# Optimization experiments

Hardware: AMD Instinct MI355X
Metric: run time of the kernel (lower is better)

Reference implementation:

```python
import jax, jax.numpy as jnp
import numpy as np

B, H, T, D, R = 2, 12, 2048, 64, 16
D_STD = D - R


def setup_inputs() -> dict:
    key = jax.random.key(0)
    ks = jax.random.split(key, 5)
    return {
        "Q": jax.random.normal(ks[0], (B, H, T, D), jnp.float32),
        "K": jax.random.normal(ks[1], (B, H, T, D), jnp.float32),
        "V": jax.random.normal(ks[2], (B, H, T, D), jnp.float32),
        "d_bias": jax.random.normal(ks[3], (B, H, T), jnp.float32),
        "W_recip": jax.random.normal(ks[4], (D, R), jnp.float32) * 0.02,
        "w_std": jnp.full((H,), 0.5, jnp.float32),
        "w_rec": jnp.full((H,), 0.3, jnp.float32),
        "w_disc": jnp.full((H,), 0.2, jnp.float32),
    }


def reference(Q, K, V, d_bias, W_recip, w_std, w_rec, w_disc):
    b, h, t, d = Q.shape
    r = W_recip.shape[1]
    d_std = d - r
    sq_std = jnp.sqrt(w_std)[None, :, None, None]  # [1,H,1,1]
    sq_rec = jnp.sqrt(w_rec)[None, :, None, None]
    Q_low = jnp.einsum("bhtd,dr->bhtr", Q, W_recip)  # [B,H,T,R]
    K_low = jnp.einsum("bhtd,dr->bhtr", K, W_recip)
    Q_aug = jnp.concatenate([sq_std * Q[..., :d_std], sq_rec * K_low], axis=-1)  # [B,H,T,D]
    K_aug = jnp.concatenate([sq_std * K[..., :d_std], sq_rec * Q_low], axis=-1)
    scale = 1.0 / jnp.sqrt(jnp.asarray(d, Q.dtype))
    scores = jnp.einsum("bhqd,bhkd->bhqk", Q_aug, K_aug) * scale  # [B,H,T,T]
    # rank-1 additive bias, broadcast over queries: bias[b,h,q,k] = w_disc[h]*d_bias[b,h,k]
    scores = scores + (w_disc[None, :, None, None] * d_bias[:, :, None, :])
    causal = jnp.tril(jnp.ones((t, t), bool))  # [T,T]
    scores = jnp.where(causal[None, None], scores, -jnp.inf)
    attn = jax.nn.softmax(scores, axis=-1)
    return jnp.einsum("bhqk,bhkd->bhqd", attn, V)
```

## Files before the change

kernel.cpp:

```cpp
#include <hip/hip_runtime.h>
#include <math.h>

#define T_SEQ 2048
#define NH    12
#define NB    2
#define BHC   (NB*NH)
#define NQT   32

typedef _Float16 half4_t __attribute__((ext_vector_type(4)));
typedef _Float16 half8_t __attribute__((ext_vector_type(8)));
typedef float    floatx4 __attribute__((ext_vector_type(4)));

__device__ __forceinline__ half8_t h8splat(_Float16 s) {
  return (half8_t){s, s, s, s, s, s, s, s};
}

__global__ __launch_bounds__(256) void prep_kernel(
    const float* __restrict__ Q, const float* __restrict__ K,
    const float* __restrict__ V, const float* __restrict__ W,
    const float* __restrict__ wstd, const float* __restrict__ wrec,
    const float* __restrict__ dbias, const float* __restrict__ wdisc,
    ushort* __restrict__ QF, ushort* __restrict__ KF, ushort* __restrict__ VF,
    float* __restrict__ B2)
{
  __shared__ __align__(16) _Float16 Qsh[64*72];
  __shared__ __align__(16) _Float16 Ksh[64*72];
  __shared__ __align__(16) _Float16 Vsh[64*72];
  __shared__ __align__(16) _Float16 Lqh[64*16];
  __shared__ __align__(16) _Float16 Lkh[64*16];

  const int tid = threadIdx.x;
  const int w = tid >> 6, lane = tid & 63;
  const int quad = lane >> 4, ln = lane & 15;
  const int bh = blockIdx.x >> 5, tblk = blockIdx.x & 31;
  const long g0 = ((long)bh * T_SEQ + tblk * 64) * 64;

  const float4* gQ = (const float4*)(Q + g0);
  const float4* gK = (const float4*)(K + g0);
  const float4* gV = (const float4*)(V + g0);
  for (int i = tid; i < 1024; i += 256) {
    int r = i >> 4, c4 = i & 15;
    float4 q = gQ[i], k = gK[i], v = gV[i];
    *(half4_t*)&Qsh[r*72 + c4*4] = (half4_t){(_Float16)q.x,(_Float16)q.y,(_Float16)q.z,(_Float16)q.w};
    *(half4_t*)&Ksh[r*72 + c4*4] = (half4_t){(_Float16)k.x,(_Float16)k.y,(_Float16)k.z,(_Float16)k.w};
    *(half4_t*)&Vsh[r*72 + c4*4] = (half4_t){(_Float16)v.x,(_Float16)v.y,(_Float16)v.z,(_Float16)v.w};
  }
  __syncthreads();

  half4_t bw[4];
#pragma unroll
  for (int dk = 0; dk < 4; dk++)
#pragma unroll
    for (int i = 0; i < 4; i++)
      bw[dk][i] = (_Float16)W[(dk*16 + quad*4 + i)*16 + ln];

  floatx4 cq = {0.f,0.f,0.f,0.f}, ck = {0.f,0.f,0.f,0.f};
#pragma unroll
  for (int dk = 0; dk < 4; dk++) {
    half4_t aq = *(const half4_t*)&Qsh[(w*16 + ln)*72 + dk*16 + quad*4];
    half4_t ak = *(const half4_t*)&Ksh[(w*16 + ln)*72 + dk*16 + quad*4];
    cq = __builtin_amdgcn_mfma_f32_16x16x16f16(aq, bw[dk], cq, 0, 0, 0);
    ck = __builtin_amdgcn_mfma_f32_16x16x16f16(ak, bw[dk], ck, 0, 0, 0);
  }
#pragma unroll
  for (int i = 0; i < 4; i++) {
    Lqh[(w*16 + quad*4 + i)*16 + ln] = (_Float16)cq[i];
    Lkh[(w*16 + quad*4 + i)*16 + ln] = (_Float16)ck[i];
  }
  __syncthreads();

  const int h = bh % NH;
  const float sstd = sqrtf(wstd[h]);
  const float srec = sqrtf(wrec[h]);
  const half8_t hq_std = h8splat((_Float16)(0.125f * sstd));
  const half8_t hk_std = h8splat((_Float16)sstd);
  const half8_t hq_rec = h8splat((_Float16)(0.125f * srec));
  const half8_t hk_rec = h8splat((_Float16)srec);

  if (tid < 64) B2[(long)bh*T_SEQ + tblk*64 + tid] =
      wdisc[h] * dbias[(long)bh*T_SEQ + tblk*64 + tid];

#pragma unroll
  for (int cc = 0; cc < 2; cc++) {
    int c = tid + cc * 256;
    {
      int lp = c & 63, dp = (c >> 6) & 1, rt = c >> 7;
      int row = rt*16 + (lp & 15);
      int d0 = dp*32 + (lp >> 4)*8;
      half8_t hq, hk;
      if (d0 < 48) {
        hq = *(const half8_t*)&Qsh[row*72 + d0] * hq_std;
        hk = *(const half8_t*)&Ksh[row*72 + d0] * hk_std;
      } else {
        hq = *(const half8_t*)&Lkh[row*16 + (d0-48)] * hq_rec;
        hk = *(const half8_t*)&Lqh[row*16 + (d0-48)] * hk_rec;
      }
      long tile16 = (long)bh*128 + tblk*4 + rt;
      ((int4*)QF)[tile16*128 + dp*64 + lp] = *(int4*)&hq;
      ((int4*)KF)[tile16*128 + dp*64 + lp] = *(int4*)&hk;
    }
    {
      int lv = c & 63, nt = (c >> 6) & 3, v2 = c >> 8;
      int d = nt*16 + (lv & 15), qv = lv >> 4;
      half8_t hv;
#pragma unroll
      for (int j = 0; j < 4; j++) {
        hv[j]   = Vsh[(v2*32 + qv*4 + j)*72 + d];
        hv[4+j] = Vsh[(v2*32 + 16 + qv*4 + j)*72 + d];
      }
      ((int4*)VF)[((long)bh*32 + tblk)*512 + (v2*4 + nt)*64 + lv] = *(int4*)&hv;
    }
  }
}

__global__ __launch_bounds__(64, 3) void flash_kernel(
    const ushort* __restrict__ QF, const ushort* __restrict__ KF,
    const ushort* __restrict__ VF, const float* __restrict__ B2,
    float* __restrict__ Out)
{
  const int lane = threadIdx.x;
  const int quad = lane >> 4, ln = lane & 15;
  const int bid = blockIdx.x;
  const int bh  = bid % BHC;
  const int t16 = 127 - bid / BHC;
  const int qrow = t16*16 + ln;
  const int ktmax = t16 >> 2;

  const ushort* gK = KF + (long)bh * 131072;
  const ushort* gV = VF + (long)bh * 131072;
  const float*  gB = B2 + (long)bh * T_SEQ;

  half8_t bq[2];
  {
    const ushort* gQ = QF + ((long)bh*128 + t16) * 1024;
    bq[0] = *(const half8_t*)(gQ + lane*8);
    bq[1] = *(const half8_t*)(gQ + 512 + lane*8);
  }

  float m_i = -1e30f, l_i = 0.f;
  floatx4 acc[4];
#pragma unroll
  for (int nt = 0; nt < 4; nt++) acc[nt] = (floatx4){0.f,0.f,0.f,0.f};

  half8_t kf[8], vf[8];
#pragma unroll
  for (int c = 0; c < 8; c++) {
    kf[c] = *(const half8_t*)(gK + c*512 + lane*8);
    vf[c] = *(const half8_t*)(gV + c*512 + lane*8);
  }

  for (int kt = 0; kt <= ktmax; kt++) {
    const long onx = (long)(kt < ktmax ? kt + 1 : kt) * 4096;

    floatx4 st[4];
#pragma unroll
    for (int mt = 0; mt < 4; mt++) {
      floatx4 c = (floatx4){0.f,0.f,0.f,0.f};
      c = __builtin_amdgcn_mfma_f32_16x16x32_f16(kf[mt*2],     bq[0], c, 0, 0, 0);
      c = __builtin_amdgcn_mfma_f32_16x16x32_f16(kf[mt*2 + 1], bq[1], c, 0, 0, 0);
      st[mt] = c;
    }
#pragma unroll
    for (int c = 0; c < 8; c++)
      kf[c] = *(const half8_t*)(gK + onx + c*512 + lane*8);

    const bool diag = (kt == ktmax);
    float rowmax = -1e30f;
#pragma unroll
    for (int mt = 0; mt < 4; mt++) {
      float4 bb = *(const float4*)(gB + kt*64 + mt*16 + quad*4);
      float bv[4] = {bb.x, bb.y, bb.z, bb.w};
#pragma unroll
      for (int i = 0; i < 4; i++) {
        float v = st[mt][i] + bv[i];
        int key = kt*64 + mt*16 + quad*4 + i;
        if (diag && key > qrow) v = -1e30f;
        st[mt][i] = v;
        rowmax = fmaxf(rowmax, v);
      }
    }
    rowmax = fmaxf(rowmax, __shfl_xor(rowmax, 16));
    rowmax = fmaxf(rowmax, __shfl_xor(rowmax, 32));
    float mnew  = fmaxf(m_i, rowmax);
    float alpha = __expf(m_i - mnew);
    float psum = 0.f;
    half4_t pa[4];
#pragma unroll
    for (int mt = 0; mt < 4; mt++)
#pragma unroll
      for (int i = 0; i < 4; i++) {
        float p = __expf(st[mt][i] - mnew);
        psum += p;
        pa[mt][i] = (_Float16)p;
      }
    psum += __shfl_xor(psum, 16);
    psum += __shfl_xor(psum, 32);
    l_i = l_i * alpha + psum;
    m_i = mnew;

    float af[4];
#pragma unroll
    for (int i = 0; i < 4; i++) af[i] = __shfl(alpha, quad*4 + i);
#pragma unroll
    for (int nt = 0; nt < 4; nt++)
#pragma unroll
      for (int i = 0; i < 4; i++) acc[nt][i] *= af[i];

#pragma unroll
    for (int v2 = 0; v2 < 2; v2++)
#pragma unroll
      for (int nt = 0; nt < 4; nt++) {
        half8_t vv = vf[v2*4 + nt];
        half4_t b0 = __builtin_shufflevector(vv, vv, 0,1,2,3);
        half4_t b1 = __builtin_shufflevector(vv, vv, 4,5,6,7);
        acc[nt] = __builtin_amdgcn_mfma_f32_16x16x16f16(pa[2*v2],   b0, acc[nt], 0, 0, 0);
        acc[nt] = __builtin_amdgcn_mfma_f32_16x16x16f16(pa[2*v2+1], b1, acc[nt], 0, 0, 0);
      }
#pragma unroll
    for (int c = 0; c < 8; c++)
      vf[c] = *(const half8_t*)(gV + onx + c*512 + lane*8);
  }

  float lr[4];
#pragma unroll
  for (int i = 0; i < 4; i++) lr[i] = 1.f / __shfl(l_i, quad*4 + i);
  const long obase = (long)bh*T_SEQ*64 + (long)(t16*16)*64;
#pragma unroll
  for (int i = 0; i < 4; i++)
#pragma unroll
    for (int nt = 0; nt < 4; nt++)
      Out[obase + (quad*4 + i)*64 + nt*16 + ln] = acc[nt][i] * lr[i];
}

extern "C" void kernel_launch(void* const* d_in, const int* in_sizes, int n_in,
                              void* d_out, int out_size, void* d_ws, size_t ws_size,
                              hipStream_t stream) {
  const float* Q     = (const float*)d_in[0];
  const float* K     = (const float*)d_in[1];
  const float* V     = (const float*)d_in[2];
  const float* dbias = (const float*)d_in[3];
  const float* W     = (const float*)d_in[4];
  const float* wstd  = (const float*)d_in[5];
  const float* wrec  = (const float*)d_in[6];
  const float* wdisc = (const float*)d_in[7];
  float* Out = (float*)d_out;

  const long NEL = (long)BHC * T_SEQ * 64;
  ushort* QF = (ushort*)d_ws;
  ushort* KF = QF + NEL;
  ushort* VF = KF + NEL;
  float*  B2 = (float*)(VF + NEL);

  prep_kernel<<<BHC * NQT, 256, 0, stream>>>(Q, K, V, W, wstd, wrec, dbias, wdisc,
                                             QF, KF, VF, B2);
  flash_kernel<<<BHC * 128, 64, 0, stream>>>(QF, KF, VF, B2, Out);
}
```

Measured before the change: 130.1 us.

## Split KV loop across two waves per block, merge softmax states, use exp2 with lazy rescale

Each flash block now runs two wavefronts that process alternating 64-key tiles, each keeping its own running max, sum and accumulator. The two partial states are merged through shared memory at the end. This doubles parallelism for each 16-row query tile to cut the serial per-wave loop latency. Separately, log2(e) is folded into the Q scale and the bias so exp2f can replace __expf. The accumulator rescale is skipped unless the row max grows by more than 8, which trades some fp16 probability headroom for fewer rescales. The change adds shared memory, a block barrier and a final merge step.

Result: slower. 339.6 us (+161.1%).

```diff
diff --git a/kernel.cpp b/kernel.cpp
--- a/kernel.cpp
+++ b/kernel.cpp
@@ -70,15 +70,16 @@
   __syncthreads();
 
   const int h = bh % NH;
+  const float LOG2E = 1.4426950408889634f;
   const float sstd = sqrtf(wstd[h]);
   const float srec = sqrtf(wrec[h]);
-  const half8_t hq_std = h8splat((_Float16)(0.125f * sstd));
+  const half8_t hq_std = h8splat((_Float16)(0.125f * sstd * LOG2E));
   const half8_t hk_std = h8splat((_Float16)sstd);
-  const half8_t hq_rec = h8splat((_Float16)(0.125f * srec));
+  const half8_t hq_rec = h8splat((_Float16)(0.125f * srec * LOG2E));
   const half8_t hk_rec = h8splat((_Float16)srec);
 
   if (tid < 64) B2[(long)bh*T_SEQ + tblk*64 + tid] =
-      wdisc[h] * dbias[(long)bh*T_SEQ + tblk*64 + tid];
+      LOG2E * wdisc[h] * dbias[(long)bh*T_SEQ + tblk*64 + tid];
 
 #pragma unroll
   for (int cc = 0; cc < 2; cc++) {
@@ -113,12 +114,18 @@
   }
 }
 
-__global__ __launch_bounds__(64, 3) void flash_kernel(
+__global__ __launch_bounds__(128, 6) void flash_kernel(
     const ushort* __restrict__ QF, const ushort* __restrict__ KF,
     const ushort* __restrict__ VF, const float* __restrict__ B2,
     float* __restrict__ Out)
 {
-  const int lane = threadIdx.x;
+  __shared__ float sm1[16];
+  __shared__ float sl1[16];
+  __shared__ float sacc1[64*16];
+
+  const int tid  = threadIdx.x;
+  const int wv   = tid >> 6;
+  const int lane = tid & 63;
   const int quad = lane >> 4, ln = lane & 15;
   const int bid = blockIdx.x;
   const int bh  = bid % BHC;
@@ -142,15 +149,17 @@
 #pragma unroll
   for (int nt = 0; nt < 4; nt++) acc[nt] = (floatx4){0.f,0.f,0.f,0.f};
 
+  const int kt0 = wv;
+  const long oo0 = (long)(kt0 <= ktmax ? kt0 : 0) * 4096;
   half8_t kf[8], vf[8];
 #pragma unroll
   for (int c = 0; c < 8; c++) {
-    kf[c] = *(const half8_t*)(gK + c*512 + lane*8);
-    vf[c] = *(const half8_t*)(gV + c*512 + lane*8);
-  }
-
-  for (int kt = 0; kt <= ktmax; kt++) {
-    const long onx = (long)(kt < ktmax ? kt + 1 : kt) * 4096;
+    kf[c] = *(const half8_t*)(gK + oo0 + c*512 + lane*8);
+    vf[c] = *(const half8_t*)(gV + oo0 + c*512 + lane*8);
+  }
+
+  for (int kt = kt0; kt <= ktmax; kt += 2) {
+    const long onx = (long)(kt + 2 <= ktmax ? kt + 2 : kt) * 4096;
 
     floatx4 st[4];
 #pragma unroll
@@ -181,30 +190,34 @@
     }
     rowmax = fmaxf(rowmax, __shfl_xor(rowmax, 16));
     rowmax = fmaxf(rowmax, __shfl_xor(rowmax, 32));
-    float mnew  = fmaxf(m_i, rowmax);
-    float alpha = __expf(m_i - mnew);
+
+    if (!__all(rowmax <= m_i + 8.f)) {
+      float mnew  = fmaxf(m_i, rowmax);
+      float alpha = exp2f(m_i - mnew);
+      float af[4];
+#pragma unroll
+      for (int i = 0; i < 4; i++) af[i] = __shfl(alpha, quad*4 + i);
+#pragma unroll
+      for (int nt = 0; nt < 4; nt++)
+#pragma unroll
+        for (int i = 0; i < 4; i++) acc[nt][i] *= af[i];
+      l_i *= alpha;
+      m_i  = mnew;
+    }
+
     float psum = 0.f;
     half4_t pa[4];
 #pragma unroll
     for (int mt = 0; mt < 4; mt++)
 #pragma unroll
       for (int i = 0; i < 4; i++) {
-        float p = __expf(st[mt][i] - mnew);
+        float p = exp2f(st[mt][i] - m_i);
         psum += p;
         pa[mt][i] = (_Float16)p;
       }
     psum += __shfl_xor(psum, 16);
     psum += __shfl_xor(psum, 32);
-    l_i = l_i * alpha + psum;
-    m_i = mnew;
-
-    float af[4];
-#pragma unroll
-    for (int i = 0; i < 4; i++) af[i] = __shfl(alpha, quad*4 + i);
-#pragma unroll
-    for (int nt = 0; nt < 4; nt++)
-#pragma unroll
-      for (int i = 0; i < 4; i++) acc[nt][i] *= af[i];
+    l_i += psum;
 
 #pragma unroll
     for (int v2 = 0; v2 < 2; v2++)
@@ -221,15 +234,39 @@
       vf[c] = *(const half8_t*)(gV + onx + c*512 + lane*8);
   }
 
-  float lr[4];
-#pragma unroll
-  for (int i = 0; i < 4; i++) lr[i] = 1.f / __shfl(l_i, quad*4 + i);
-  const long obase = (long)bh*T_SEQ*64 + (long)(t16*16)*64;
-#pragma unroll
-  for (int i = 0; i < 4; i++)
+  if (wv == 1) {
+    if (quad == 0) { sm1[ln] = m_i; sl1[ln] = l_i; }
 #pragma unroll
     for (int nt = 0; nt < 4; nt++)
-      Out[obase + (quad*4 + i)*64 + nt*16 + ln] = acc[nt][i] * lr[i];
+#pragma unroll
+      for (int i = 0; i < 4; i++)
+        sacc1[lane*16 + nt*4 + i] = acc[nt][i];
+  }
+  __syncthreads();
+  if (wv == 0) {
+    const float m1  = sm1[ln];
+    const float l1v = sl1[ln];
+    const float mm  = fmaxf(m_i, m1);
+    const float w0  = exp2f(m_i - mm);
+    const float w1  = exp2f(m1  - mm);
+    const float lm  = l_i * w0 + l1v * w1;
+    float w0r[4], w1r[4], lr[4];
+#pragma unroll
+    for (int i = 0; i < 4; i++) {
+      w0r[i] = __shfl(w0, quad*4 + i);
+      w1r[i] = __shfl(w1, quad*4 + i);
+      lr[i]  = 1.f / __shfl(lm, quad*4 + i);
+    }
+    const long obase = (long)bh*T_SEQ*64 + (long)(t16*16)*64;
+#pragma unroll
+    for (int i = 0; i < 4; i++)
+#pragma unroll
+      for (int nt = 0; nt < 4; nt++) {
+        float4 a1 = *(const float4*)&sacc1[lane*16 + nt*4];
+        Out[obase + (quad*4 + i)*64 + nt*16 + ln] =
+            (acc[nt][i]*w0r[i] + ((const float*)&a1)[i]*w1r[i]) * lr[i];
+      }
+  }
 }
 
 extern "C" void kernel_launch(void* const* d_in, const int* in_sizes, int n_in,
@@ -253,5 +290,5 @@
 
   prep_kernel<<<BHC * NQT, 256, 0, stream>>>(Q, K, V, W, wstd, wrec, dbias, wdisc,
                                              QF, KF, VF, B2);
-  flash_kernel<<<BHC * 128, 64, 0, stream>>>(QF, KF, VF, B2, Out);
-}
+  flash_kernel<<<BHC * 128, 128, 0, stream>>>(QF, KF, VF, B2, Out);
+}
```

## Share K/V tiles across four waves via LDS double-buffering, use exp2 and lazy rescale

Applied to the files above, without the earlier changes.

The flash kernel now runs four waves per block, each handling one 16-row query tile of a 64-row group. K/V tiles are staged once per block into double-buffered LDS with global_load_lds, so four waves share each load instead of each wave fetching its own from global memory. The log2(e) factor is folded into the Q scaling and bias in prep, so the softmax uses exp2f. The running-max rescale is skipped unless some row's max grows by more than 8 (in log2 units), which trims work in exchange for fp16 overflow risk when the max is stale. Per-iteration __syncthreads adds synchronisation, and waves in a block now share the same causal loop length, so the wave on the lowest query tile does extra masked work.

Result: slower. 136.5 us (+5.0%).

```diff
diff --git a/kernel.cpp b/kernel.cpp
--- a/kernel.cpp
+++ b/kernel.cpp
@@ -13,6 +13,12 @@
 
 __device__ __forceinline__ half8_t h8splat(_Float16 s) {
   return (half8_t){s, s, s, s, s, s, s, s};
+}
+
+__device__ __forceinline__ void gload_lds16(const void* g, void* l) {
+  __builtin_amdgcn_global_load_lds(
+      (const __attribute__((address_space(1))) unsigned int*)g,
+      (__attribute__((address_space(3))) unsigned int*)l, 16, 0, 0);
 }
 
 __global__ __launch_bounds__(256) void prep_kernel(
@@ -70,15 +76,16 @@
   __syncthreads();
 
   const int h = bh % NH;
+  const float LOG2E = 1.4426950408889634f;
   const float sstd = sqrtf(wstd[h]);
   const float srec = sqrtf(wrec[h]);
-  const half8_t hq_std = h8splat((_Float16)(0.125f * sstd));
+  const half8_t hq_std = h8splat((_Float16)(0.125f * sstd * LOG2E));
   const half8_t hk_std = h8splat((_Float16)sstd);
-  const half8_t hq_rec = h8splat((_Float16)(0.125f * srec));
+  const half8_t hq_rec = h8splat((_Float16)(0.125f * srec * LOG2E));
   const half8_t hk_rec = h8splat((_Float16)srec);
 
   if (tid < 64) B2[(long)bh*T_SEQ + tblk*64 + tid] =
-      wdisc[h] * dbias[(long)bh*T_SEQ + tblk*64 + tid];
+      LOG2E * wdisc[h] * dbias[(long)bh*T_SEQ + tblk*64 + tid];
 
 #pragma unroll
   for (int cc = 0; cc < 2; cc++) {
@@ -113,18 +120,23 @@
   }
 }
 
-__global__ __launch_bounds__(64, 3) void flash_kernel(
+__global__ __launch_bounds__(256, 3) void flash_kernel(
     const ushort* __restrict__ QF, const ushort* __restrict__ KF,
     const ushort* __restrict__ VF, const float* __restrict__ B2,
     float* __restrict__ Out)
 {
-  const int lane = threadIdx.x;
+  __shared__ __align__(16) _Float16 KV[2][2][4096];
+
+  const int tid  = threadIdx.x;
+  const int wv   = tid >> 6;
+  const int lane = tid & 63;
   const int quad = lane >> 4, ln = lane & 15;
   const int bid = blockIdx.x;
   const int bh  = bid % BHC;
-  const int t16 = 127 - bid / BHC;
+  const int p   = 31 - bid / BHC;
+  const int t16 = 4*p + wv;
   const int qrow = t16*16 + ln;
-  const int ktmax = t16 >> 2;
+  const int ktmax = p;
 
   const ushort* gK = KF + (long)bh * 131072;
   const ushort* gV = VF + (long)bh * 131072;
@@ -142,16 +154,31 @@
 #pragma unroll
   for (int nt = 0; nt < 4; nt++) acc[nt] = (floatx4){0.f,0.f,0.f,0.f};
 
-  half8_t kf[8], vf[8];
-#pragma unroll
-  for (int c = 0; c < 8; c++) {
-    kf[c] = *(const half8_t*)(gK + c*512 + lane*8);
-    vf[c] = *(const half8_t*)(gV + c*512 + lane*8);
-  }
+  auto STAGE = [&](int nbuf, int kt) {
+    const long tb = (long)kt * 4096;
+#pragma unroll
+    for (int s = 0; s < 4; s++) {
+      const int c = wv + s*4;
+      const ushort* src = (c < 8 ? gK + tb + c*512 : gV + tb + (c-8)*512) + lane*8;
+      gload_lds16(src, &KV[nbuf][c>>3][(c&7)*512]);
+    }
+  };
+  STAGE(0, 0);
 
   for (int kt = 0; kt <= ktmax; kt++) {
-    const long onx = (long)(kt < ktmax ? kt + 1 : kt) * 4096;
-
+    const int cur = kt & 1;
+    __syncthreads();
+    if (kt < ktmax) STAGE(cur ^ 1, kt + 1);
+
+    float4 bb[4];
+#pragma unroll
+    for (int mt = 0; mt < 4; mt++)
+      bb[mt] = *(const float4*)(gB + kt*64 + mt*16 + quad*4);
+
+    half8_t kf[8];
+#pragma unroll
+    for (int c = 0; c < 8; c++)
+      kf[c] = *(const half8_t*)&KV[cur][0][c*512 + lane*8];
     floatx4 st[4];
 #pragma unroll
     for (int mt = 0; mt < 4; mt++) {
@@ -160,65 +187,60 @@
       c = __builtin_amdgcn_mfma_f32_16x16x32_f16(kf[mt*2 + 1], bq[1], c, 0, 0, 0);
       st[mt] = c;
     }
-#pragma unroll
-    for (int c = 0; c < 8; c++)
-      kf[c] = *(const half8_t*)(gK + onx + c*512 + lane*8);
 
     const bool diag = (kt == ktmax);
     float rowmax = -1e30f;
 #pragma unroll
-    for (int mt = 0; mt < 4; mt++) {
-      float4 bb = *(const float4*)(gB + kt*64 + mt*16 + quad*4);
-      float bv[4] = {bb.x, bb.y, bb.z, bb.w};
+    for (int mt = 0; mt < 4; mt++)
 #pragma unroll
       for (int i = 0; i < 4; i++) {
-        float v = st[mt][i] + bv[i];
+        float v = st[mt][i] + ((const float*)&bb[mt])[i];
         int key = kt*64 + mt*16 + quad*4 + i;
         if (diag && key > qrow) v = -1e30f;
         st[mt][i] = v;
         rowmax = fmaxf(rowmax, v);
       }
-    }
     rowmax = fmaxf(rowmax, __shfl_xor(rowmax, 16));
     rowmax = fmaxf(rowmax, __shfl_xor(rowmax, 32));
-    float mnew  = fmaxf(m_i, rowmax);
-    float alpha = __expf(m_i - mnew);
+
+    if (!__all(rowmax <= m_i + 8.f)) {
+      float mnew  = fmaxf(m_i, rowmax);
+      float alpha = exp2f(m_i - mnew);
+      float af[4];
+#pragma unroll
+      for (int i = 0; i < 4; i++) af[i] = __shfl(alpha, quad*4 + i);
+#pragma unroll
+      for (int nt = 0; nt < 4; nt++)
+#pragma unroll
+        for (int i = 0; i < 4; i++) acc[nt][i] *= af[i];
+      l_i *= alpha;
+      m_i  = mnew;
+    }
+
     float psum = 0.f;
     half4_t pa[4];
 #pragma unroll
     for (int mt = 0; mt < 4; mt++)
 #pragma unroll
       for (int i = 0; i < 4; i++) {
-        float p = __expf(st[mt][i] - mnew);
-        psum += p;
-        pa[mt][i] = (_Float16)p;
+        float pv = exp2f(st[mt][i] - m_i);
+        psum += pv;
+        pa[mt][i] = (_Float16)pv;
       }
     psum += __shfl_xor(psum, 16);
     psum += __shfl_xor(psum, 32);
-    l_i = l_i * alpha + psum;
-    m_i = mnew;
-
-    float af[4];
-#pragma unroll
-    for (int i = 0; i < 4; i++) af[i] = __shfl(alpha, quad*4 + i);
-#pragma unroll
-    for (int nt = 0; nt < 4; nt++)
-#pragma unroll
-      for (int i = 0; i < 4; i++) acc[nt][i] *= af[i];
+    l_i += psum;
 
 #pragma unroll
     for (int v2 = 0; v2 < 2; v2++)
 #pragma unroll
       for (int nt = 0; nt < 4; nt++) {
-        half8_t vv = vf[v2*4 + nt];
+        half8_t vv = *(const half8_t*)&KV[cur][1][(v2*4 + nt)*512 + lane*8];
         half4_t b0 = __builtin_shufflevector(vv, vv, 0,1,2,3);
         half4_t b1 = __builtin_shufflevector(vv, vv, 4,5,6,7);
         acc[nt] = __builtin_amdgcn_mfma_f32_16x16x16f16(pa[2*v2],   b0, acc[nt], 0, 0, 0);
         acc[nt] = __builtin_amdgcn_mfma_f32_16x16x16f16(pa[2*v2+1], b1, acc[nt], 0, 0, 0);
       }
-#pragma unroll
-    for (int c = 0; c < 8; c++)
-      vf[c] = *(const half8_t*)(gV + onx + c*512 + lane*8);
   }
 
   float lr[4];
@@ -253,5 +275,5 @@
 
   prep_kernel<<<BHC * NQT, 256, 0, stream>>>(Q, K, V, W, wstd, wrec, dbias, wdisc,
                                              QF, KF, VF, B2);
-  flash_kernel<<<BHC * 128, 64, 0, stream>>>(QF, KF, VF, B2, Out);
-}
+  flash_kernel<<<BHC * 32, 256, 0, stream>>>(QF, KF, VF, B2, Out);
+}
```

## Split long causal rows across key chunks with merge kernel, exp2 softmax and lazy rescale

Applied to the files above, without the earlier changes.

Splits each query tile's key range into chunks of up to 8 key tiles, so long causal rows become several blocks (320 per head instead of 128). Each block writes unnormalized partial outputs plus running max and sum, and a new merge kernel combines them. This balances the triangular workload and adds parallelism. It also folds log2(e) into the Q scales and the bias so softmax can use exp2, seeds the MFMA accumulator with the bias, and skips rescaling while the new max stays within 8 of the old one. The cost is an extra kernel launch and a round trip of partial results through global memory. It also raises the occupancy hint from 3 to 4.

After: 141.4 us. +8.7%, slower.

```diff
diff --git a/kernel.cpp b/kernel.cpp
--- a/kernel.cpp
+++ b/kernel.cpp
@@ -70,15 +70,16 @@
   __syncthreads();
 
   const int h = bh % NH;
+  const float LOG2E = 1.4426950408889634f;
   const float sstd = sqrtf(wstd[h]);
   const float srec = sqrtf(wrec[h]);
-  const half8_t hq_std = h8splat((_Float16)(0.125f * sstd));
+  const half8_t hq_std = h8splat((_Float16)(0.125f * sstd * LOG2E));
   const half8_t hk_std = h8splat((_Float16)sstd);
-  const half8_t hq_rec = h8splat((_Float16)(0.125f * srec));
+  const half8_t hq_rec = h8splat((_Float16)(0.125f * srec * LOG2E));
   const half8_t hk_rec = h8splat((_Float16)srec);
 
   if (tid < 64) B2[(long)bh*T_SEQ + tblk*64 + tid] =
-      wdisc[h] * dbias[(long)bh*T_SEQ + tblk*64 + tid];
+      LOG2E * wdisc[h] * dbias[(long)bh*T_SEQ + tblk*64 + tid];
 
 #pragma unroll
   for (int cc = 0; cc < 2; cc++) {
@@ -113,18 +114,30 @@
   }
 }
 
-__global__ __launch_bounds__(64, 3) void flash_kernel(
+__global__ __launch_bounds__(64, 4) void flash_kernel(
     const ushort* __restrict__ QF, const ushort* __restrict__ KF,
     const ushort* __restrict__ VF, const float* __restrict__ B2,
-    float* __restrict__ Out)
+    float* __restrict__ PP)
 {
   const int lane = threadIdx.x;
   const int quad = lane >> 4, ln = lane & 15;
   const int bid = blockIdx.x;
   const int bh  = bid % BHC;
-  const int t16 = 127 - bid / BHC;
+  int rem = 319 - bid / BHC;
+
+  int p = 0;
+#pragma unroll 1
+  for (p = 0; p < 32; p++) {
+    int cnt = 4 * ((p >> 3) + 1);
+    if (rem < cnt) break;
+    rem -= cnt;
+  }
+  const int t16 = 4*p + (rem & 3);
+  const int s   = rem >> 2;
+  const int ktmax = p;
+  const int s0 = s*8;
+  const int s1 = min(s0 + 7, ktmax);
   const int qrow = t16*16 + ln;
-  const int ktmax = t16 >> 2;
 
   const ushort* gK = KF + (long)bh * 131072;
   const ushort* gV = VF + (long)bh * 131072;
@@ -145,17 +158,18 @@
   half8_t kf[8], vf[8];
 #pragma unroll
   for (int c = 0; c < 8; c++) {
-    kf[c] = *(const half8_t*)(gK + c*512 + lane*8);
-    vf[c] = *(const half8_t*)(gV + c*512 + lane*8);
-  }
-
-  for (int kt = 0; kt <= ktmax; kt++) {
-    const long onx = (long)(kt < ktmax ? kt + 1 : kt) * 4096;
+    kf[c] = *(const half8_t*)(gK + (long)s0*4096 + c*512 + lane*8);
+    vf[c] = *(const half8_t*)(gV + (long)s0*4096 + c*512 + lane*8);
+  }
+
+  for (int kt = s0; kt <= s1; kt++) {
+    const long onx = (long)(kt < s1 ? kt + 1 : kt) * 4096;
 
     floatx4 st[4];
 #pragma unroll
     for (int mt = 0; mt < 4; mt++) {
-      floatx4 c = (floatx4){0.f,0.f,0.f,0.f};
+      float4 bb = *(const float4*)(gB + kt*64 + mt*16 + quad*4);
+      floatx4 c = (floatx4){bb.x, bb.y, bb.z, bb.w};
       c = __builtin_amdgcn_mfma_f32_16x16x32_f16(kf[mt*2],     bq[0], c, 0, 0, 0);
       c = __builtin_amdgcn_mfma_f32_16x16x32_f16(kf[mt*2 + 1], bq[1], c, 0, 0, 0);
       st[mt] = c;
@@ -164,47 +178,51 @@
     for (int c = 0; c < 8; c++)
       kf[c] = *(const half8_t*)(gK + onx + c*512 + lane*8);
 
-    const bool diag = (kt == ktmax);
+    if (kt == ktmax) {
+#pragma unroll
+      for (int mt = 0; mt < 4; mt++)
+#pragma unroll
+        for (int i = 0; i < 4; i++) {
+          int key = kt*64 + mt*16 + quad*4 + i;
+          if (key > qrow) st[mt][i] = -1e30f;
+        }
+    }
     float rowmax = -1e30f;
 #pragma unroll
-    for (int mt = 0; mt < 4; mt++) {
-      float4 bb = *(const float4*)(gB + kt*64 + mt*16 + quad*4);
-      float bv[4] = {bb.x, bb.y, bb.z, bb.w};
-#pragma unroll
-      for (int i = 0; i < 4; i++) {
-        float v = st[mt][i] + bv[i];
-        int key = kt*64 + mt*16 + quad*4 + i;
-        if (diag && key > qrow) v = -1e30f;
-        st[mt][i] = v;
-        rowmax = fmaxf(rowmax, v);
-      }
-    }
+    for (int mt = 0; mt < 4; mt++)
+      rowmax = fmaxf(rowmax,
+                     fmaxf(fmaxf(st[mt][0], st[mt][1]),
+                           fmaxf(st[mt][2], st[mt][3])));
     rowmax = fmaxf(rowmax, __shfl_xor(rowmax, 16));
     rowmax = fmaxf(rowmax, __shfl_xor(rowmax, 32));
-    float mnew  = fmaxf(m_i, rowmax);
-    float alpha = __expf(m_i - mnew);
+
+    if (!__all(rowmax <= m_i + 8.f)) {
+      float mnew  = fmaxf(m_i, rowmax);
+      float alpha = exp2f(m_i - mnew);
+      float af[4];
+#pragma unroll
+      for (int i = 0; i < 4; i++) af[i] = __shfl(alpha, quad*4 + i);
+#pragma unroll
+      for (int nt = 0; nt < 4; nt++)
+#pragma unroll
+        for (int i = 0; i < 4; i++) acc[nt][i] *= af[i];
+      l_i *= alpha;
+      m_i  = mnew;
+    }
+
     float psum = 0.f;
     half4_t pa[4];
 #pragma unroll
     for (int mt = 0; mt < 4; mt++)
 #pragma unroll
       for (int i = 0; i < 4; i++) {
-        float p = __expf(st[mt][i] - mnew);
-        psum += p;
-        pa[mt][i] = (_Float16)p;
+        float pv = exp2f(st[mt][i] - m_i);
+        psum += pv;
+        pa[mt][i] = (_Float16)pv;
       }
     psum += __shfl_xor(psum, 16);
     psum += __shfl_xor(psum, 32);
-    l_i = l_i * alpha + psum;
-    m_i = mnew;
-
-    float af[4];
-#pragma unroll
-    for (int i = 0; i < 4; i++) af[i] = __shfl(alpha, quad*4 + i);
-#pragma unroll
-    for (int nt = 0; nt < 4; nt++)
-#pragma unroll
-      for (int i = 0; i < 4; i++) acc[nt][i] *= af[i];
+    l_i += psum;
 
 #pragma unroll
     for (int v2 = 0; v2 < 2; v2++)
@@ -221,15 +239,59 @@
       vf[c] = *(const half8_t*)(gV + onx + c*512 + lane*8);
   }
 
-  float lr[4];
-#pragma unroll
-  for (int i = 0; i < 4; i++) lr[i] = 1.f / __shfl(l_i, quad*4 + i);
-  const long obase = (long)bh*T_SEQ*64 + (long)(t16*16)*64;
+  float* pb = PP + ((long)((bh*128 + t16)*4 + s)) * 1088;
 #pragma unroll
   for (int i = 0; i < 4; i++)
 #pragma unroll
     for (int nt = 0; nt < 4; nt++)
-      Out[obase + (quad*4 + i)*64 + nt*16 + ln] = acc[nt][i] * lr[i];
+      pb[(quad*4 + i)*64 + nt*16 + ln] = acc[nt][i];
+  if (quad == 0) {
+    pb[1024 + ln] = m_i;
+    pb[1040 + ln] = l_i;
+  }
+}
+
+__global__ __launch_bounds__(256) void merge_kernel(
+    const float* __restrict__ PP, float* __restrict__ Out)
+{
+  const int tid = threadIdx.x, wv = tid >> 6, lane = tid & 63;
+  const int gidx = blockIdx.x * 4 + wv;
+  const int bh = gidx % BHC, t16 = gidx / BHC;
+  const int scnt = (t16 >> 5) + 1;
+  const float* base = PP + ((long)(bh*128 + t16)*4) * 1088;
+  const int colg = (lane & 15) * 4;
+  const int r0   = lane >> 4;
+
+  float mm[4] = {-1e30f, -1e30f, -1e30f, -1e30f};
+  for (int sI = 0; sI < scnt; sI++)
+#pragma unroll
+    for (int j = 0; j < 4; j++)
+      mm[j] = fmaxf(mm[j], base[sI*1088 + 1024 + (r0 + 4*j)]);
+
+  float L[4] = {0.f, 0.f, 0.f, 0.f};
+  floatx4 O[4];
+#pragma unroll
+  for (int j = 0; j < 4; j++) O[j] = (floatx4){0.f,0.f,0.f,0.f};
+
+  for (int sI = 0; sI < scnt; sI++)
+#pragma unroll
+    for (int j = 0; j < 4; j++) {
+      const int row = r0 + 4*j;
+      const float w = exp2f(base[sI*1088 + 1024 + row] - mm[j]);
+      L[j] += base[sI*1088 + 1040 + row] * w;
+      const float4 a = *(const float4*)&base[sI*1088 + row*64 + colg];
+      O[j][0] += a.x * w;  O[j][1] += a.y * w;
+      O[j][2] += a.z * w;  O[j][3] += a.w * w;
+    }
+
+  const long obase = (long)bh*T_SEQ*64 + (long)t16*16*64;
+#pragma unroll
+  for (int j = 0; j < 4; j++) {
+    const float inv = 1.f / L[j];
+    const int row = r0 + 4*j;
+    float4 o = {O[j][0]*inv, O[j][1]*inv, O[j][2]*inv, O[j][3]*inv};
+    *(float4*)&Out[obase + row*64 + colg] = o;
+  }
 }
 
 extern "C" void kernel_launch(void* const* d_in, const int* in_sizes, int n_in,
@@ -250,8 +312,10 @@
   ushort* KF = QF + NEL;
   ushort* VF = KF + NEL;
   float*  B2 = (float*)(VF + NEL);
+  float*  PP = B2 + (long)BHC * T_SEQ;
 
   prep_kernel<<<BHC * NQT, 256, 0, stream>>>(Q, K, V, W, wstd, wrec, dbias, wdisc,
                                              QF, KF, VF, B2);
-  flash_kernel<<<BHC * 128, 64, 0, stream>>>(QF, KF, VF, B2, Out);
-}
+  flash_kernel<<<BHC * 320, 64, 0, stream>>>(QF, KF, VF, B2, PP);
+  merge_kernel<<<768, 256, 0, stream>>>(PP, Out);
+}
```
